# Kernel tuning notes

Measured on AMD Instinct MI355X. Metric: run time of the kernel, lower is better.

## Reference

```python
import jax, jax.numpy as jnp
import numpy as np

V, E, TH, SRC = 50000, 128, 512, 512
B, S, OOV = 256, 512, 100
UNK = 1
NEG_INF = jnp.float32(-jnp.inf)


def setup_inputs() -> dict:
    key = jax.random.key(0)
    ks = jax.random.split(key, 16)
    sc = 0.02
    inp = {
        'embedding': jax.random.normal(ks[0], (V, E), jnp.float32) * sc,
        'W_ih': jax.random.normal(ks[1], (4 * TH, E + TH + SRC), jnp.float32) * sc,
        'W_hh': jax.random.normal(ks[2], (4 * TH, TH), jnp.float32) * sc,
        'b_ih': jnp.zeros((4 * TH,), jnp.float32),
        'b_hh': jnp.zeros((4 * TH,), jnp.float32),
        'W_attn': jax.random.normal(ks[3], (SRC, TH), jnp.float32) * sc,
        'W_out': jax.random.normal(ks[4], (TH, SRC + TH), jnp.float32) * sc,
        'b_out': jnp.zeros((TH,), jnp.float32),
        'W_copy': jax.random.normal(ks[5], (TH, SRC), jnp.float32) * sc,
        'W_incopy': jax.random.normal(ks[6], (TH, SRC), jnp.float32) * sc,
        'W_gen': jax.random.normal(ks[7], (V, TH), jnp.float32) * sc,
        'encoder_output': jax.random.normal(ks[8], (B, S, SRC), jnp.float32),
        'prev_context_state': jax.random.normal(ks[9], (B, TH), jnp.float32),
        'h0': jax.random.normal(ks[10], (B, TH), jnp.float32),
        'c0': jax.random.normal(ks[11], (B, TH), jnp.float32),
        'prev_output_tokens': jax.random.randint(ks[12], (B, 1), 0, V, jnp.int64 if jax.config.jax_enable_x64 else jnp.int32),
        'src_tokens_with_oov': jax.random.randint(ks[13], (B, S), 0, V + OOV, jnp.int64 if jax.config.jax_enable_x64 else jnp.int32),
    }
    lengths = jax.random.randint(ks[14], (B, 1), S // 2, S + 1)
    inp['encoder_padding_mask'] = jnp.arange(S)[None, :] >= lengths  # B x S bool
    return inp


def reference(embedding, W_ih, W_hh, b_ih, b_hh, W_attn, W_out, b_out,
              W_copy, W_incopy, W_gen, encoder_output, prev_context_state,
              h0, c0, prev_output_tokens, src_tokens_with_oov, encoder_padding_mask):
    # ---- attentive-read copy state ----
    match = prev_output_tokens == src_tokens_with_oov            # B x S
    maskf = match[..., None].astype(encoder_output.dtype)        # B x S x 1
    agg = jnp.tanh(jnp.einsum('bsd,hd->bsh', maskf * encoder_output, W_incopy))  # B S TH
    has_match = jnp.any(match, axis=1, keepdims=True)            # B x 1
    fill_mask = has_match & match                                # B x S (as in original)
    in_copy_logit = jnp.einsum('bsh,bh->bs', agg, prev_context_state)
    in_copy_logit = jnp.where(fill_mask, NEG_INF, in_copy_logit)
    in_copy_w = jax.nn.softmax(in_copy_logit, axis=1)            # B x S
    copy_state = jnp.einsum('bs,bsd->bd', in_copy_w, encoder_output)  # B x SRC

    # ---- embed prev token (OOV -> UNK) ----
    tok = jnp.where(prev_output_tokens[:, 0] >= V, UNK, prev_output_tokens[:, 0])
    src_embed = embedding[tok]                                   # B x E

    # ---- one-step LSTM (input_feeding) ----
    x = jnp.concatenate([src_embed, prev_context_state, copy_state], axis=-1)
    gates = x @ W_ih.T + b_ih + h0 @ W_hh.T + b_hh               # B x 4TH
    i, f, g, o = jnp.split(gates, 4, axis=-1)
    c1 = jax.nn.sigmoid(f) * c0 + jax.nn.sigmoid(i) * jnp.tanh(g)
    h1 = jax.nn.sigmoid(o) * jnp.tanh(c1)                        # B x TH

    # ---- general attention ----
    q = h1 @ W_attn.T                                            # B x SRC
    attn_logits = jnp.einsum('bd,bsd->bs', q, encoder_output)
    attn_logits = jnp.where(encoder_padding_mask, NEG_INF, attn_logits)
    attn_w = jax.nn.softmax(attn_logits, axis=1)
    context = jnp.einsum('bs,bsd->bd', attn_w, encoder_output)   # B x SRC
    attn_out = jnp.tanh(jnp.concatenate([context, h1], axis=-1) @ W_out.T + b_out)  # B x TH

    # ---- generate + copy distribution ----
    gen_logits = attn_out @ W_gen.T                              # B x V
    gen_logits = jnp.concatenate([gen_logits, jnp.zeros((gen_logits.shape[0], OOV), gen_logits.dtype)], axis=1)
    copy_seq = jnp.einsum('bsh,bh->bs', jnp.tanh(jnp.einsum('bsd,hd->bsh', encoder_output, W_copy)), attn_out)
    copy_seq = jnp.exp(jnp.where(encoder_padding_mask, NEG_INF, copy_seq))  # B x S
    rows = jnp.arange(copy_seq.shape[0])[:, None]
    copy_vocab = jnp.zeros((copy_seq.shape[0], V + OOV), copy_seq.dtype).at[rows, src_tokens_with_oov].add(copy_seq)

    total = jnp.exp(gen_logits) + copy_vocab
    total_prob = jnp.log(total / jnp.sum(total, axis=1, keepdims=True))
    return total_prob, attn_out, h1, c1
```

## Files before the change

### kernel.cpp

```cpp
#include <hip/hip_runtime.h>
#include <hip/hip_bf16.h>
#include <math.h>

#define V_ 50000
#define OOV_ 100
#define VX_ 50100
#define B_ 256
#define S_ 512
#define TH_ 512
#define SRC_ 512
#define KXH 1664

#define ATT_OFF ((size_t)B_ * VX_)
#define H1_OFF (ATT_OFF + (size_t)B_ * TH_)
#define C1_OFF (H1_OFF + (size_t)B_ * TH_)

typedef float f32x4 __attribute__((ext_vector_type(4)));
typedef short s16x8 __attribute__((ext_vector_type(8)));

__device__ __forceinline__ unsigned short f2bf(float f) {
    unsigned int u = __float_as_uint(f);
    u += 0x7FFFu + ((u >> 16) & 1u);
    return (unsigned short)(u >> 16);
}
__device__ __forceinline__ unsigned int pk2bf(float x, float y) {
    __hip_bfloat162 h = __float22bfloat162_rn(make_float2(x, y));
    return *reinterpret_cast<unsigned int*>(&h);
}
__device__ __forceinline__ float fast_tanh(float x) {
    return 1.0f - 2.0f / (__expf(2.0f * x) + 1.0f);
}
__device__ __forceinline__ float sigm(float x) { return 1.0f / (1.0f + __expf(-x)); }

__device__ __forceinline__ bool get_mask(const void* m, int flag, size_t idx) {
    return flag ? (((const unsigned char*)m)[idx] != 0)
                : (((const int*)m)[idx] != 0);
}

__device__ __forceinline__ void mfma_acc(f32x4& c, s16x8 a, s16x8 b) {
    c = __builtin_amdgcn_mfma_f32_16x16x32_bf16(a, b, c, 0, 0, 0);
}


__device__ __forceinline__ void stage_bf16(const unsigned short* src, int ld,
                                           int row0, int k0, unsigned char* ldsbase) {
    const int tid = threadIdx.x;
    const int w = tid >> 6, lane = tid & 63;
#pragma unroll
    for (int jj = 0; jj < 2; ++jj) {
        const int qq = w * 2 + jj;
        const int rowl = qq * 8 + (lane >> 3);
        const int su = (lane & 7) ^ (rowl & 7);
        const unsigned short* g = src + (size_t)(row0 + rowl) * ld + k0 + su * 8;
        __builtin_amdgcn_global_load_lds(
            (const __attribute__((address_space(1))) void*)g,
            (__attribute__((address_space(3))) void*)(ldsbase + qq * 1024), 16, 0, 0);
    }
}

__device__ __forceinline__ void stage_bf16_128(const unsigned short* src, int ld,
                                               int k0, unsigned char* ldsbase) {
    const int tid = threadIdx.x;
    const int w = tid >> 6, lane = tid & 63;
#pragma unroll
    for (int jj = 0; jj < 4; ++jj) {
        const int qq = w * 4 + jj;
        const int rowl = qq * 8 + (lane >> 3);
        const int su = (lane & 7) ^ (rowl & 7);
        const unsigned short* g = src + (size_t)rowl * ld + k0 + su * 8;
        __builtin_amdgcn_global_load_lds(
            (const __attribute__((address_space(1))) void*)g,
            (__attribute__((address_space(3))) void*)(ldsbase + qq * 1024), 16, 0, 0);
    }
}

__device__ __forceinline__ void stage_f32(const float* src, int ld, int row0, int k0,
                                          int rowmax, unsigned char* ldsbase) {
    const int tid = threadIdx.x;
#pragma unroll
    for (int it = 0; it < 4; ++it) {
        const int p = it * 256 + tid;
        const int row = p >> 4;
        const int u4 = p & 15;
        int gr = row0 + row;
        gr = gr > rowmax ? rowmax : gr;
        const float4 v = *(const float4*)(src + (size_t)gr * ld + k0 + u4 * 4);
        *(uint2*)(ldsbase + row * 128 + ((u4 * 8) ^ ((row & 7) << 4))) =
            make_uint2(pk2bf(v.x, v.y), pk2bf(v.z, v.w));
    }
}

__device__ __forceinline__ void compute64(const unsigned char* Ab, const unsigned char* Bb,
                                          f32x4 acc[4]) {
    const int tid = threadIdx.x;
    const int w = tid >> 6, lane = tid & 63, lq = lane >> 4, lr = lane & 15;
#pragma unroll
    for (int ks = 0; ks < 2; ++ks) {
        const int kb = ks * 64 + lq * 16;
        const int ar = w * 16 + lr;
        s16x8 a = *(const s16x8*)(Ab + ar * 128 + (kb ^ ((ar & 7) << 4)));
#pragma unroll
        for (int ns = 0; ns < 4; ++ns) {
            const int br = ns * 16 + lr;
            s16x8 b = *(const s16x8*)(Bb + br * 128 + (kb ^ ((br & 7) << 4)));
            mfma_acc(acc[ns], a, b);
        }
    }
}

template <bool BF32>
__device__ __forceinline__ void gemm_main(const unsigned short* A, int lda, const void* Bp,
                                          int ldb, int nkc, int kbase, int rowmaxB, int m0,
                                          int n0, unsigned char* smem, f32x4 acc[4]) {
#pragma unroll
    for (int i = 0; i < 4; ++i) acc[i] = f32x4{0.f, 0.f, 0.f, 0.f};
    unsigned char* const A0 = smem;
    unsigned char* const B0 = smem + 8192;
    for (int kc = 0; kc < nkc; ++kc) {
        const int k0 = kbase + kc * 64;
        __syncthreads();
        stage_bf16(A, lda, m0, k0, A0);
        if (BF32) stage_f32((const float*)Bp, ldb, n0, k0, rowmaxB, B0);
        else      stage_bf16((const unsigned short*)Bp, ldb, n0, k0, B0);
        __syncthreads();
        compute64(A0, B0, acc);
    }
}


__global__ __launch_bounds__(256) void k_pre(const float* enc, const int* stok, const int* ptok,
                                             float* cs_sum, int* cs_cnt, unsigned short* ebf,
                                             int do_cvt, float* logit, float* rowsum,
                                             const void* maskp, int* flag, float* out,
                                             const float* W_ih, const float* W_hh,
                                             const float* W_copy, unsigned short* Wg,
                                             unsigned short* Wcb, float* gates) {
    const int bid = blockIdx.x, tid = threadIdx.x;
    if (bid < 1024) {
        __shared__ float comb[512];
        __shared__ int cc[2];
        const int b = bid >> 2, chunk = bid & 3;
        const int h = tid >> 7, d0 = (tid & 127) * 4;
        const int prev = ptok[b];
        const float* base = enc + ((size_t)b * S_ + chunk * 128) * SRC_;
        const int* st = stok + b * S_ + chunk * 128;
        unsigned short* eb = ebf + ((size_t)b * S_ + chunk * 128) * SRC_;
        float a0 = 0.f, a1 = 0.f, a2 = 0.f, a3 = 0.f;
        int cnt = 0;
        for (int s2 = 0; s2 < 64; ++s2) {
            const int s = s2 * 2 + h;
            const float4 v = *(const float4*)(base + (size_t)s * SRC_ + d0);
            if (st[s] != prev) { a0 += v.x; a1 += v.y; a2 += v.z; a3 += v.w; ++cnt; }
            if (do_cvt) {
                *(uint2*)(eb + (size_t)s * SRC_ + d0) =
                    make_uint2(pk2bf(v.x, v.y), pk2bf(v.z, v.w));
            }
        }
        if (h == 0) {
            comb[d0] = a0; comb[d0 + 1] = a1; comb[d0 + 2] = a2; comb[d0 + 3] = a3;
            if (tid == 0) cc[0] = cnt;
        }
        __syncthreads();
        if (h == 1) {
            comb[d0] += a0; comb[d0 + 1] += a1; comb[d0 + 2] += a2; comb[d0 + 3] += a3;
            if (tid == 128) cc[1] = cnt;
        }
        __syncthreads();
        cs_sum[(size_t)bid * SRC_ + tid] = comb[tid];
        cs_sum[(size_t)bid * SRC_ + 256 + tid] = comb[256 + tid];
        if (tid == 0) cs_cnt[bid] = cc[0] + cc[1];
    } else if (bid < 1536) {
        logit[(bid - 1024) * 256 + tid] = 0.f;
    } else if (bid == 1536) {
        rowsum[tid] = (float)OOV_;
    } else if (bid == 1537) {
        __shared__ int sfl;
        if (tid == 0) sfl = 0;
        __syncthreads();
        const uint4* m4 = (const uint4*)maskp;
        unsigned int ev = 0;
        for (int i = tid; i < (B_ * S_) / 16; i += 256) {
            const uint4 u = m4[i];
            ev |= (u.x | u.y | u.z | u.w) & 0xFFFFFF00u;
        }
        if (ev) atomicOr(&sfl, 1);
        __syncthreads();
        if (tid == 0) *flag = sfl;
    } else if (bid < 1638) {
        const int p = (bid - 1538) * 256 + tid;
        if (p < B_ * OOV_) {
            const int b = p / OOV_, j = p - b * OOV_;
            out[(size_t)b * VX_ + V_ + j] = 1.0f;
        }
    } else if (bid < 2150) {
        const int NWG = 2048 * KXH;
        const int NTOT4 = (NWG + 512 * 512) / 4;
        for (int i4 = (bid - 1638) * 256 + tid; i4 < NTOT4; i4 += 512 * 256) {
            const int e = i4 * 4;
            float4 v;
            unsigned short* dst;
            if (e < NWG) {
                const int r = e / KXH, c = e - r * KXH;
                v = (c < 1152) ? *(const float4*)(W_ih + (size_t)r * 1152 + c)
                               : *(const float4*)(W_hh + (size_t)r * 512 + (c - 1152));
                dst = Wg + e;
            } else {
                v = *(const float4*)(W_copy + (e - NWG));
                dst = Wcb + (e - NWG);
            }
            *(uint2*)dst = make_uint2(pk2bf(v.x, v.y), pk2bf(v.z, v.w));
        }
    } else {
        ((float4*)gates)[(bid - 2150) * 256 + tid] = make_float4(0.f, 0.f, 0.f, 0.f);
    }
}

__global__ __launch_bounds__(256) void k_cs_final(const float* cs_sum, const int* cs_cnt,
                                                  const float* embedding, const int* ptok,
                                                  const float* pcs, const float* h0,
                                                  unsigned short* xh) {
    const int b = blockIdx.x, tid = threadIdx.x;
    const int cnt = cs_cnt[b * 4] + cs_cnt[b * 4 + 1] + cs_cnt[b * 4 + 2] + cs_cnt[b * 4 + 3];
    const float inv = 1.f / (float)cnt;
    unsigned short* row = xh + (size_t)b * KXH;
    for (int d = tid; d < 512; d += 256) {
        float s = cs_sum[(size_t)(b * 4 + 0) * SRC_ + d] + cs_sum[(size_t)(b * 4 + 1) * SRC_ + d] +
                  cs_sum[(size_t)(b * 4 + 2) * SRC_ + d] + cs_sum[(size_t)(b * 4 + 3) * SRC_ + d];
        row[640 + d] = f2bf(s * inv);
        row[128 + d] = f2bf(pcs[b * 512 + d]);
        row[1152 + d] = f2bf(h0[b * 512 + d]);
    }
    if (tid < 128) {
        int tk = ptok[b];
        if (tk >= V_) tk = 1;
        row[tid] = f2bf(embedding[(size_t)tk * 128 + tid]);
    }
}

__global__ __launch_bounds__(256) void k_gates(const unsigned short* xh, const unsigned short* Wg,
                                               float* gates) {
    __shared__ __align__(16) unsigned char smem[16384];
    f32x4 acc[4];
    const int m0 = blockIdx.x * 64, n0 = blockIdx.y * 64;
    const int kb = blockIdx.z ? 832 : 0;
    gemm_main<false>(xh, KXH, Wg, KXH, 13, kb, 2047, m0, n0, smem, acc);
    const int tid = threadIdx.x, w = tid >> 6, lane = tid & 63, lq = lane >> 4, lr = lane & 15;
#pragma unroll
    for (int ns = 0; ns < 4; ++ns) {
        const int n = n0 + ns * 16 + lr;
#pragma unroll
        for (int r = 0; r < 4; ++r) {
            const int m = m0 + w * 16 + lq * 4 + r;
            atomicAdd(&gates[(size_t)m * 2048 + n], acc[ns][r]);
        }
    }
}

__global__ __launch_bounds__(256) void k_lstm(const float* gates, const float* b_ih,
                                              const float* b_hh, const float* c0, float* out,
                                              unsigned short* h1b) {
    const int idx = blockIdx.x * 256 + threadIdx.x;
    const int b = idx >> 9, h = idx & 511;
    const float gi = gates[(size_t)b * 2048 + h] + b_ih[h] + b_hh[h];
    const float gf = gates[(size_t)b * 2048 + 512 + h] + b_ih[512 + h] + b_hh[512 + h];
    const float gg = gates[(size_t)b * 2048 + 1024 + h] + b_ih[1024 + h] + b_hh[1024 + h];
    const float go = gates[(size_t)b * 2048 + 1536 + h] + b_ih[1536 + h] + b_hh[1536 + h];
    const float c1 = sigm(gf) * c0[idx] + sigm(gi) * fast_tanh(gg);
    const float h1 = sigm(go) * fast_tanh(c1);
    out[H1_OFF + idx] = h1;
    out[C1_OFF + idx] = c1;
    h1b[idx] = f2bf(h1);
}

__global__ __launch_bounds__(256) void k_q(const unsigned short* h1b, const float* W_attn,
                                           float* qbuf) {
    __shared__ __align__(16) unsigned char smem[16384];
    f32x4 acc[4];
    const int m0 = blockIdx.x * 64, n0 = blockIdx.y * 64;
    gemm_main<true>(h1b, 512, W_attn, 512, 8, 0, 511, m0, n0, smem, acc);
    const int tid = threadIdx.x, w = tid >> 6, lane = tid & 63, lq = lane >> 4, lr = lane & 15;
#pragma unroll
    for (int ns = 0; ns < 4; ++ns) {
        const int n = n0 + ns * 16 + lr;
#pragma unroll
        for (int r = 0; r < 4; ++r)
            qbuf[(size_t)(m0 + w * 16 + lq * 4 + r) * 512 + n] = acc[ns][r];
    }
}

__global__ __launch_bounds__(256) void k_attn2(const float* enc, const unsigned short* ebf,
                                               const int use_ebf, const float* qv,
                                               const void* maskp, const int* flagp,
                                               float* parts, float* md) {
    const int chunk = blockIdx.x, b = blockIdx.y;
    const int tid = threadIdx.x, w = tid >> 6, lane = tid & 63;
    const int flag = *flagp;
    float q0[8];
    {
        const float4 t0 = *(const float4*)(qv + b * 512 + lane * 8);
        const float4 t1 = *(const float4*)(qv + b * 512 + lane * 8 + 4);
        q0[0] = t0.x; q0[1] = t0.y; q0[2] = t0.z; q0[3] = t0.w;
        q0[4] = t1.x; q0[5] = t1.y; q0[6] = t1.z; q0[7] = t1.w;
    }
    float M = -INFINITY, den = 0.f;
    float cv[8] = {0.f, 0.f, 0.f, 0.f, 0.f, 0.f, 0.f, 0.f};
    const int s0 = chunk * 128 + w * 32;
    for (int i = 0; i < 32; ++i) {
        const int s = s0 + i;
        if (get_mask(maskp, flag, (size_t)b * S_ + s)) continue;
        float v[8];
        if (use_ebf) {
            const uint4 u = *(const uint4*)(ebf + ((size_t)b * S_ + s) * 512 + lane * 8);
            v[0] = __uint_as_float(u.x << 16);
            v[1] = __uint_as_float(u.x & 0xffff0000u);
            v[2] = __uint_as_float(u.y << 16);
            v[3] = __uint_as_float(u.y & 0xffff0000u);
            v[4] = __uint_as_float(u.z << 16);
            v[5] = __uint_as_float(u.z & 0xffff0000u);
            v[6] = __uint_as_float(u.w << 16);
            v[7] = __uint_as_float(u.w & 0xffff0000u);
        } else {
            const float4 t0 = *(const float4*)(enc + ((size_t)b * S_ + s) * 512 + lane * 8);
            const float4 t1 = *(const float4*)(enc + ((size_t)b * S_ + s) * 512 + lane * 8 + 4);
            v[0] = t0.x; v[1] = t0.y; v[2] = t0.z; v[3] = t0.w;
            v[4] = t1.x; v[5] = t1.y; v[6] = t1.z; v[7] = t1.w;
        }
        float a = 0.f;
#pragma unroll
        for (int j = 0; j < 8; ++j) a += q0[j] * v[j];
        a += __shfl_xor(a, 1);
        a += __shfl_xor(a, 2);
        a += __shfl_xor(a, 4);
        a += __shfl_xor(a, 8);
        a += __shfl_xor(a, 16);
        a += __shfl_xor(a, 32);
        const float nM = fmaxf(M, a);
        const float sc = __expf(M - nM);
        const float p = __expf(a - nM);
        den = den * sc + p;
#pragma unroll
        for (int j = 0; j < 8; ++j) cv[j] = cv[j] * sc + p * v[j];
        M = nM;
    }
    const int part = chunk * 4 + w;
    float* pp = parts + ((size_t)part * B_ + b) * 512 + lane * 8;
    *(float4*)pp = make_float4(cv[0], cv[1], cv[2], cv[3]);
    *(float4*)(pp + 4) = make_float4(cv[4], cv[5], cv[6], cv[7]);
    if (lane == 0) {
        md[(part * B_ + b) * 2] = M;
        md[(part * B_ + b) * 2 + 1] = den;
    }
}

__global__ __launch_bounds__(256) void k_merge16(const float* parts, const float* md,
                                                 const unsigned short* h1b, unsigned short* ch) {
    const int b = blockIdx.x, tid = threadIdx.x;
    float Ms[16], Ds[16], M = -INFINITY;
#pragma unroll
    for (int jj = 0; jj < 16; ++jj) {
        Ms[jj] = md[(jj * B_ + b) * 2];
        Ds[jj] = md[(jj * B_ + b) * 2 + 1];
        M = fmaxf(M, Ms[jj]);
    }
    float den = 0.f, sc[16];
#pragma unroll
    for (int jj = 0; jj < 16; ++jj) {
        sc[jj] = __expf(Ms[jj] - M);
        den += Ds[jj] * sc[jj];
    }
    const float inv = 1.f / den;
    for (int d = tid; d < 512; d += 256) {
        float c = 0.f;
#pragma unroll
        for (int jj = 0; jj < 16; ++jj) c += parts[((size_t)jj * B_ + b) * 512 + d] * sc[jj];
        ch[(size_t)b * 1024 + d] = f2bf(c * inv);
    }
    ch[(size_t)b * 1024 + 512 + tid] = h1b[b * 512 + tid];
    ch[(size_t)b * 1024 + 512 + 256 + tid] = h1b[b * 512 + 256 + tid];
}

__global__ __launch_bounds__(256) void k_attnout(const unsigned short* ch, const float* W_out,
                                                 const float* b_out, float* out,
                                                 unsigned short* aob) {
    __shared__ __align__(16) unsigned char smem[16384];
    f32x4 acc[4];
    const int m0 = blockIdx.x * 64, n0 = blockIdx.y * 64;
    gemm_main<true>(ch, 1024, W_out, 1024, 16, 0, 511, m0, n0, smem, acc);
    const int tid = threadIdx.x, w = tid >> 6, lane = tid & 63, lq = lane >> 4, lr = lane & 15;
#pragma unroll
    for (int ns = 0; ns < 4; ++ns) {
        const int n = n0 + ns * 16 + lr;
        const float bb = b_out[n];
#pragma unroll
        for (int r = 0; r < 4; ++r) {
            const int m = m0 + w * 16 + lq * 4 + r;
            const float t = fast_tanh(acc[ns][r] + bb);
            out[ATT_OFF + (size_t)m * 512 + n] = t;
            aob[(size_t)m * 512 + n] = f2bf(t);
        }
    }
}

__global__ __launch_bounds__(256) void k_gen(const unsigned short* aob, const float* W_gen,
                                             float* out, float* rowsum) {
    __shared__ __align__(16) unsigned char smem[16384];
    f32x4 acc[4];
    const int d = blockIdx.x;
    const int l = (d & 7) * 391 + (d >> 3);
    const int m0 = (l & 3) * 64;
    const int n0 = (l >> 2) * 64;
    gemm_main<true>(aob, 512, W_gen, 512, 8, 0, V_ - 1, m0, n0, smem, acc);
    const int tid = threadIdx.x, w = tid >> 6, lane = tid & 63, lq = lane >> 4, lr = lane & 15;
    float rp[4] = {0.f, 0.f, 0.f, 0.f};
#pragma unroll
    for (int ns = 0; ns < 4; ++ns) {
        const int n = n0 + ns * 16 + lr;
        if (n < V_) {
#pragma unroll
            for (int r = 0; r < 4; ++r) {
                const float v = __expf(acc[ns][r]);
                out[(size_t)(m0 + w * 16 + lq * 4 + r) * VX_ + n] = v;
                rp[r] += v;
            }
        }
    }
#pragma unroll
    for (int r = 0; r < 4; ++r) {
        rp[r] += __shfl_xor(rp[r], 1, 16);
        rp[r] += __shfl_xor(rp[r], 2, 16);
        rp[r] += __shfl_xor(rp[r], 4, 16);
        rp[r] += __shfl_xor(rp[r], 8, 16);
    }
    if (lr == 0) {
#pragma unroll
        for (int r = 0; r < 4; ++r) atomicAdd(&rowsum[m0 + w * 16 + lq * 4 + r], rp[r]);
    }
}

__global__ __launch_bounds__(256) void k_copyseq_bf(const unsigned short* ebf,
                                                    const unsigned short* Wcb,
                                                    const float* ao, const void* maskp,
                                                    const int* flagp, float* logit) {
    const int d = blockIdx.x;
    const int l = (d & 7) * 512 + (d >> 3);
    const int n0 = (l & 3) * 128;
    const int mt = l >> 2;
    const int m0 = mt * 128;
    const int b = mt >> 2;
    if (get_mask(maskp, *flagp, (size_t)b * S_ + (m0 & 511))) return;
    __shared__ __align__(16) unsigned char smem[65536];
    unsigned char* const A0 = smem;
    unsigned char* const A1 = smem + 16384;
    unsigned char* const B0 = smem + 32768;
    unsigned char* const B1 = smem + 49152;
    const int tid = threadIdx.x;
    const int w = tid >> 6, lane = tid & 63;
    const int wm = w >> 1, wn = w & 1, lq = lane >> 4, lr = lane & 15;
    const unsigned short* Asrc = ebf + (size_t)m0 * 512;
    const unsigned short* Bsrc = Wcb + (size_t)n0 * 512;

    f32x4 acc[4][4];
#pragma unroll
    for (int mi = 0; mi < 4; ++mi)
#pragma unroll
        for (int ni = 0; ni < 4; ++ni) acc[mi][ni] = f32x4{0.f, 0.f, 0.f, 0.f};

    stage_bf16_128(Asrc, 512, 0, A0);
    stage_bf16_128(Bsrc, 512, 0, B0);

    for (int kc = 0; kc < 8; ++kc) {
        __syncthreads();
        const unsigned char* Ac = (kc & 1) ? A1 : A0;
        const unsigned char* Bc = (kc & 1) ? B1 : B0;
        if (kc < 7) {
            stage_bf16_128(Asrc, 512, (kc + 1) * 64, (kc & 1) ? A0 : A1);
            stage_bf16_128(Bsrc, 512, (kc + 1) * 64, (kc & 1) ? B0 : B1);
        }
#pragma unroll
        for (int ks = 0; ks < 2; ++ks) {
            const int kb = ks * 64 + lq * 16;
            s16x8 afr[4], bfr[4];
#pragma unroll
            for (int mi = 0; mi < 4; ++mi) {
                const int ar = wm * 64 + mi * 16 + lr;
                afr[mi] = *(const s16x8*)(Ac + ar * 128 + (kb ^ ((ar & 7) << 4)));
            }
#pragma unroll
            for (int ni = 0; ni < 4; ++ni) {
                const int br = wn * 64 + ni * 16 + lr;
                bfr[ni] = *(const s16x8*)(Bc + br * 128 + (kb ^ ((br & 7) << 4)));
            }
#pragma unroll
            for (int mi = 0; mi < 4; ++mi)
#pragma unroll
                for (int ni = 0; ni < 4; ++ni) mfma_acc(acc[mi][ni], afr[mi], bfr[ni]);
        }
    }

    float aow[4];
#pragma unroll
    for (int ni = 0; ni < 4; ++ni) aow[ni] = ao[b * 512 + n0 + wn * 64 + ni * 16 + lr];
#pragma unroll
    for (int mi = 0; mi < 4; ++mi) {
#pragma unroll
        for (int r = 0; r < 4; ++r) {
            float p = 0.f;
#pragma unroll
            for (int ni = 0; ni < 4; ++ni) p += fast_tanh(acc[mi][ni][r]) * aow[ni];
            p += __shfl_xor(p, 1, 16);
            p += __shfl_xor(p, 2, 16);
            p += __shfl_xor(p, 4, 16);
            p += __shfl_xor(p, 8, 16);
            if (lr == 0)
                atomicAdd(&logit[(size_t)m0 + wm * 64 + mi * 16 + lq * 4 + r], p);
        }
    }
}

__global__ __launch_bounds__(256) void k_copyseq(const float* enc, const unsigned short* Wcb,
                                                 const float* ao, const void* maskp,
                                                 const int* flagp, float* logit) {
    const int m0 = blockIdx.x * 128;
    const int n0 = blockIdx.y * 128;
    const int b = blockIdx.x >> 2;
    if (get_mask(maskp, *flagp, (size_t)b * S_ + (m0 & 511))) return;
    __shared__ __align__(16) unsigned char smem[32768];
    unsigned char* const A0 = smem;
    unsigned char* const B0 = smem + 16384;
    const int tid = threadIdx.x;
    const int w = tid >> 6, lane = tid & 63;
    const int wm = w >> 1, wn = w & 1, lq = lane >> 4, lr = lane & 15;
    const float* Asrc = enc + (size_t)m0 * 512;

    f32x4 acc[4][4];
#pragma unroll
    for (int mi = 0; mi < 4; ++mi)
#pragma unroll
        for (int ni = 0; ni < 4; ++ni) acc[mi][ni] = f32x4{0.f, 0.f, 0.f, 0.f};

    const int arow_t = tid >> 3, au_t = tid & 7;
    for (int kc = 0; kc < 8; ++kc) {
        __syncthreads();
        const int k0 = kc * 64;
#pragma unroll
        for (int it = 0; it < 4; ++it) {
            const int row = arow_t + it * 32;
            const float* g = Asrc + (size_t)row * 512 + k0 + au_t * 8;
            const float4 v0 = *(const float4*)g;
            const float4 v1 = *(const float4*)(g + 4);
            uint4 pk;
            pk.x = pk2bf(v0.x, v0.y);
            pk.y = pk2bf(v0.z, v0.w);
            pk.z = pk2bf(v1.x, v1.y);
            pk.w = pk2bf(v1.z, v1.w);
            *(uint4*)(A0 + row * 128 + ((au_t * 16) ^ ((row & 7) << 4))) = pk;
        }
        stage_bf16_128(Wcb + (size_t)n0 * 512, 512, k0, B0);
        __syncthreads();
#pragma unroll
        for (int ks = 0; ks < 2; ++ks) {
            const int kb = ks * 64 + lq * 16;
            s16x8 afr[4], bfr[4];
#pragma unroll
            for (int mi = 0; mi < 4; ++mi) {
                const int ar = wm * 64 + mi * 16 + lr;
                afr[mi] = *(const s16x8*)(A0 + ar * 128 + (kb ^ ((ar & 7) << 4)));
            }
#pragma unroll
            for (int ni = 0; ni < 4; ++ni) {
                const int br = wn * 64 + ni * 16 + lr;
                bfr[ni] = *(const s16x8*)(B0 + br * 128 + (kb ^ ((br & 7) << 4)));
            }
#pragma unroll
            for (int mi = 0; mi < 4; ++mi)
#pragma unroll
                for (int ni = 0; ni < 4; ++ni) mfma_acc(acc[mi][ni], afr[mi], bfr[ni]);
        }
    }

    float aow[4];
#pragma unroll
    for (int ni = 0; ni < 4; ++ni) aow[ni] = ao[b * 512 + n0 + wn * 64 + ni * 16 + lr];
#pragma unroll
    for (int mi = 0; mi < 4; ++mi) {
#pragma unroll
        for (int r = 0; r < 4; ++r) {
            float p = 0.f;
#pragma unroll
            for (int ni = 0; ni < 4; ++ni) p += fast_tanh(acc[mi][ni][r]) * aow[ni];
            p += __shfl_xor(p, 1, 16);
            p += __shfl_xor(p, 2, 16);
            p += __shfl_xor(p, 4, 16);
            p += __shfl_xor(p, 8, 16);
            if (lr == 0)
                atomicAdd(&logit[(size_t)m0 + wm * 64 + mi * 16 + lq * 4 + r], p);
        }
    }
}

__global__ __launch_bounds__(256) void k_scatter(const float* logit, const int* stok,
                                                 const void* maskp, const int* flagp,
                                                 float* out, float* rowsum) {
    const int idx = blockIdx.x * 256 + threadIdx.x;
    const int b = idx >> 9;
    const int flag = *flagp;
    float v = 0.f;
    if (!get_mask(maskp, flag, idx)) {
        v = __expf(logit[idx]);
        atomicAdd(&out[(size_t)b * VX_ + stok[idx]], v);
    }
    float s = v;
#pragma unroll
    for (int o = 1; o < 64; o <<= 1) s += __shfl_xor(s, o, 64);
    if ((threadIdx.x & 63) == 0) atomicAdd(&rowsum[b], s);
}

__global__ __launch_bounds__(256) void k_final(float* out, const float* rowsum) {
    const int b = blockIdx.y;
    const float ls = __logf(rowsum[b]);
    int v = blockIdx.x * 1024 + threadIdx.x;
#pragma unroll
    for (int i = 0; i < 4; ++i, v += 256) {
        if (v < VX_) {
            const size_t o = (size_t)b * VX_ + v;
            out[o] = __logf(out[o]) - ls;
        }
    }
}


extern "C" void kernel_launch(void* const* d_in, const int* in_sizes, int n_in, void* d_out,
                              int out_size, void* d_ws, size_t ws_size, hipStream_t stream) {
    const float* embedding = (const float*)d_in[0];
    const float* W_ih = (const float*)d_in[1];
    const float* W_hh = (const float*)d_in[2];
    const float* b_ih = (const float*)d_in[3];
    const float* b_hh = (const float*)d_in[4];
    const float* W_attn = (const float*)d_in[5];
    const float* W_out = (const float*)d_in[6];
    const float* b_out = (const float*)d_in[7];
    const float* W_copy = (const float*)d_in[8];
    const float* W_gen = (const float*)d_in[10];
    const float* enc = (const float*)d_in[11];
    const float* pcs = (const float*)d_in[12];
    const float* h0 = (const float*)d_in[13];
    const float* c0 = (const float*)d_in[14];
    const int* ptok = (const int*)d_in[15];
    const int* stok = (const int*)d_in[16];
    const void* maskp = d_in[17];
    float* out = (float*)d_out;

    char* ws = (char*)d_ws;
    size_t off = 0;
    auto alloc = [&](size_t bytes) {
        size_t o = off;
        off += (bytes + 255) & ~(size_t)255;
        return o;
    };
    int* flag = (int*)(ws + alloc(4));
    float* rowsum = (float*)(ws + alloc(B_ * 4));
    float* cs_sum = (float*)(ws + alloc((size_t)1024 * SRC_ * 4));
    int* cs_cnt = (int*)(ws + alloc(1024 * 4));
    unsigned short* xh = (unsigned short*)(ws + alloc((size_t)B_ * KXH * 2));
    unsigned short* Wg = (unsigned short*)(ws + alloc((size_t)2048 * KXH * 2));
    unsigned short* Wcb = (unsigned short*)(ws + alloc((size_t)512 * 512 * 2));
    float* gates = (float*)(ws + alloc((size_t)B_ * 2048 * 4));
    unsigned short* h1b = (unsigned short*)(ws + alloc((size_t)B_ * 512 * 2));
    float* qbuf = (float*)(ws + alloc((size_t)B_ * 512 * 4));
    float* parts = (float*)(ws + alloc((size_t)16 * B_ * 512 * 4));
    float* md = (float*)(ws + alloc((size_t)16 * B_ * 2 * 4));
    unsigned short* ch = (unsigned short*)(ws + alloc((size_t)B_ * 1024 * 2));
    unsigned short* aob = (unsigned short*)(ws + alloc((size_t)B_ * 512 * 2));
    float* logit = (float*)(ws + alloc((size_t)B_ * S_ * 4));
    const size_t ebf_bytes = (size_t)B_ * S_ * SRC_ * 2;
    const int use_ebf = (off + ebf_bytes <= ws_size) ? 1 : 0;
    unsigned short* ebf = (unsigned short*)(ws + off);
    (void)n_in; (void)in_sizes; (void)out_size;

    hipLaunchKernelGGL(k_pre, dim3(2662), dim3(256), 0, stream, enc, stok, ptok, cs_sum, cs_cnt,
                       ebf, use_ebf, logit, rowsum, maskp, flag, out, W_ih, W_hh, W_copy, Wg,
                       Wcb, gates);
    hipLaunchKernelGGL(k_cs_final, dim3(256), dim3(256), 0, stream, cs_sum, cs_cnt, embedding,
                       ptok, pcs, h0, xh);
    hipLaunchKernelGGL(k_gates, dim3(4, 32, 2), dim3(256), 0, stream, xh, Wg, gates);
    hipLaunchKernelGGL(k_lstm, dim3(512), dim3(256), 0, stream, gates, b_ih, b_hh, c0, out, h1b);
    hipLaunchKernelGGL(k_q, dim3(4, 8), dim3(256), 0, stream, h1b, W_attn, qbuf);
    hipLaunchKernelGGL(k_attn2, dim3(4, 256), dim3(256), 0, stream, enc, ebf, use_ebf, qbuf,
                       maskp, flag, parts, md);
    hipLaunchKernelGGL(k_merge16, dim3(256), dim3(256), 0, stream, parts, md, h1b, ch);
    hipLaunchKernelGGL(k_attnout, dim3(4, 8), dim3(256), 0, stream, ch, W_out, b_out, out, aob);
    hipLaunchKernelGGL(k_gen, dim3(3128), dim3(256), 0, stream, aob, W_gen, out, rowsum);
    if (use_ebf) {
        hipLaunchKernelGGL(k_copyseq_bf, dim3(4096), dim3(256), 0, stream, ebf, Wcb,
                           out + ATT_OFF, maskp, flag, logit);
    } else {
        hipLaunchKernelGGL(k_copyseq, dim3(1024, 4), dim3(256), 0, stream, enc, Wcb,
                           out + ATT_OFF, maskp, flag, logit);
    }
    hipLaunchKernelGGL(k_scatter, dim3(512), dim3(256), 0, stream, logit, stok, maskp, flag,
                       out, rowsum);
    hipLaunchKernelGGL(k_final, dim3(49, 256), dim3(256), 0, stream, out, rowsum);
}
```

Baseline: 454.1 us.

## Fuse attention merge into one kernel and co-launch gen and copy GEMMs

Attention read is done by one 1024-thread block per batch row, which merges the 16 partial softmax states in LDS instead of writing partials to global memory and running a separate merge kernel. The generation GEMM and the copy-sequence GEMM are combined into one launch with block-index dispatch so the two can overlap on the GPU. The final log-normalize kernel is vectorized to float4. In exchange, attention parallelism drops to 256 blocks, and all tail blocks reserve 64KB of LDS, which may reduce occupancy for the gen part.

```diff
diff --git a/kernel.cpp b/kernel.cpp
--- a/kernel.cpp
+++ b/kernel.cpp
@@ -288,11 +288,13 @@
     }
 }
 
-__global__ __launch_bounds__(256) void k_attn2(const float* enc, const unsigned short* ebf,
-                                               const int use_ebf, const float* qv,
-                                               const void* maskp, const int* flagp,
-                                               float* parts, float* md) {
-    const int chunk = blockIdx.x, b = blockIdx.y;
+__global__ __launch_bounds__(1024) void k_attn3(const float* enc, const unsigned short* ebf,
+                                                const int use_ebf, const float* qv,
+                                                const void* maskp, const int* flagp,
+                                                const unsigned short* h1b, unsigned short* ch) {
+    __shared__ float plds[16][512];
+    __shared__ float mdl[16][2];
+    const int b = blockIdx.x;
     const int tid = threadIdx.x, w = tid >> 6, lane = tid & 63;
     const int flag = *flagp;
     float q0[8];
@@ -304,7 +306,7 @@
     }
     float M = -INFINITY, den = 0.f;
     float cv[8] = {0.f, 0.f, 0.f, 0.f, 0.f, 0.f, 0.f, 0.f};
-    const int s0 = chunk * 128 + w * 32;
+    const int s0 = w * 32;
     for (int i = 0; i < 32; ++i) {
         const int s = s0 + i;
         if (get_mask(maskp, flag, (size_t)b * S_ + s)) continue;
@@ -342,41 +344,25 @@
         for (int j = 0; j < 8; ++j) cv[j] = cv[j] * sc + p * v[j];
         M = nM;
     }
-    const int part = chunk * 4 + w;
-    float* pp = parts + ((size_t)part * B_ + b) * 512 + lane * 8;
-    *(float4*)pp = make_float4(cv[0], cv[1], cv[2], cv[3]);
-    *(float4*)(pp + 4) = make_float4(cv[4], cv[5], cv[6], cv[7]);
-    if (lane == 0) {
-        md[(part * B_ + b) * 2] = M;
-        md[(part * B_ + b) * 2 + 1] = den;
-    }
-}
-
-__global__ __launch_bounds__(256) void k_merge16(const float* parts, const float* md,
-                                                 const unsigned short* h1b, unsigned short* ch) {
-    const int b = blockIdx.x, tid = threadIdx.x;
-    float Ms[16], Ds[16], M = -INFINITY;
-#pragma unroll
-    for (int jj = 0; jj < 16; ++jj) {
-        Ms[jj] = md[(jj * B_ + b) * 2];
-        Ds[jj] = md[(jj * B_ + b) * 2 + 1];
-        M = fmaxf(M, Ms[jj]);
-    }
-    float den = 0.f, sc[16];
-#pragma unroll
-    for (int jj = 0; jj < 16; ++jj) {
-        sc[jj] = __expf(Ms[jj] - M);
-        den += Ds[jj] * sc[jj];
-    }
-    const float inv = 1.f / den;
-    for (int d = tid; d < 512; d += 256) {
-        float c = 0.f;
-#pragma unroll
-        for (int jj = 0; jj < 16; ++jj) c += parts[((size_t)jj * B_ + b) * 512 + d] * sc[jj];
-        ch[(size_t)b * 1024 + d] = f2bf(c * inv);
-    }
-    ch[(size_t)b * 1024 + 512 + tid] = h1b[b * 512 + tid];
-    ch[(size_t)b * 1024 + 512 + 256 + tid] = h1b[b * 512 + 256 + tid];
+    if (lane == 0) { mdl[w][0] = M; mdl[w][1] = den; }
+    *(float4*)&plds[w][lane * 8] = make_float4(cv[0], cv[1], cv[2], cv[3]);
+    *(float4*)&plds[w][lane * 8 + 4] = make_float4(cv[4], cv[5], cv[6], cv[7]);
+    __syncthreads();
+    if (tid < 512) {
+        float Mg = -INFINITY;
+#pragma unroll
+        for (int j = 0; j < 16; ++j) Mg = fmaxf(Mg, mdl[j][0]);
+        float deng = 0.f, c = 0.f;
+#pragma unroll
+        for (int j = 0; j < 16; ++j) {
+            const float sc = __expf(mdl[j][0] - Mg);
+            deng += mdl[j][1] * sc;
+            c += plds[j][tid] * sc;
+        }
+        ch[(size_t)b * 1024 + tid] = f2bf(c / deng);
+    } else {
+        ch[(size_t)b * 1024 + tid] = h1b[b * 512 + (tid - 512)];
+    }
 }
 
 __global__ __launch_bounds__(256) void k_attnout(const unsigned short* ch, const float* W_out,
@@ -401,118 +387,118 @@
     }
 }
 
-__global__ __launch_bounds__(256) void k_gen(const unsigned short* aob, const float* W_gen,
-                                             float* out, float* rowsum) {
-    __shared__ __align__(16) unsigned char smem[16384];
-    f32x4 acc[4];
-    const int d = blockIdx.x;
-    const int l = (d & 7) * 391 + (d >> 3);
-    const int m0 = (l & 3) * 64;
-    const int n0 = (l >> 2) * 64;
-    gemm_main<true>(aob, 512, W_gen, 512, 8, 0, V_ - 1, m0, n0, smem, acc);
-    const int tid = threadIdx.x, w = tid >> 6, lane = tid & 63, lq = lane >> 4, lr = lane & 15;
-    float rp[4] = {0.f, 0.f, 0.f, 0.f};
-#pragma unroll
-    for (int ns = 0; ns < 4; ++ns) {
-        const int n = n0 + ns * 16 + lr;
-        if (n < V_) {
-#pragma unroll
-            for (int r = 0; r < 4; ++r) {
-                const float v = __expf(acc[ns][r]);
-                out[(size_t)(m0 + w * 16 + lq * 4 + r) * VX_ + n] = v;
-                rp[r] += v;
-            }
-        }
-    }
-#pragma unroll
-    for (int r = 0; r < 4; ++r) {
-        rp[r] += __shfl_xor(rp[r], 1, 16);
-        rp[r] += __shfl_xor(rp[r], 2, 16);
-        rp[r] += __shfl_xor(rp[r], 4, 16);
-        rp[r] += __shfl_xor(rp[r], 8, 16);
-    }
-    if (lr == 0) {
-#pragma unroll
-        for (int r = 0; r < 4; ++r) atomicAdd(&rowsum[m0 + w * 16 + lq * 4 + r], rp[r]);
-    }
-}
-
-__global__ __launch_bounds__(256) void k_copyseq_bf(const unsigned short* ebf,
-                                                    const unsigned short* Wcb,
-                                                    const float* ao, const void* maskp,
-                                                    const int* flagp, float* logit) {
-    const int d = blockIdx.x;
-    const int l = (d & 7) * 512 + (d >> 3);
-    const int n0 = (l & 3) * 128;
-    const int mt = l >> 2;
-    const int m0 = mt * 128;
-    const int b = mt >> 2;
-    if (get_mask(maskp, *flagp, (size_t)b * S_ + (m0 & 511))) return;
+__global__ __launch_bounds__(256) void k_tail(const unsigned short* ebf,
+                                              const unsigned short* Wcb, const float* ao,
+                                              const unsigned short* aob, const float* W_gen,
+                                              const void* maskp, const int* flagp, float* out,
+                                              float* logit, float* rowsum) {
     __shared__ __align__(16) unsigned char smem[65536];
-    unsigned char* const A0 = smem;
-    unsigned char* const A1 = smem + 16384;
-    unsigned char* const B0 = smem + 32768;
-    unsigned char* const B1 = smem + 49152;
     const int tid = threadIdx.x;
     const int w = tid >> 6, lane = tid & 63;
-    const int wm = w >> 1, wn = w & 1, lq = lane >> 4, lr = lane & 15;
-    const unsigned short* Asrc = ebf + (size_t)m0 * 512;
-    const unsigned short* Bsrc = Wcb + (size_t)n0 * 512;
-
-    f32x4 acc[4][4];
-#pragma unroll
-    for (int mi = 0; mi < 4; ++mi)
-#pragma unroll
-        for (int ni = 0; ni < 4; ++ni) acc[mi][ni] = f32x4{0.f, 0.f, 0.f, 0.f};
-
-    stage_bf16_128(Asrc, 512, 0, A0);
-    stage_bf16_128(Bsrc, 512, 0, B0);
-
-    for (int kc = 0; kc < 8; ++kc) {
-        __syncthreads();
-        const unsigned char* Ac = (kc & 1) ? A1 : A0;
-        const unsigned char* Bc = (kc & 1) ? B1 : B0;
-        if (kc < 7) {
-            stage_bf16_128(Asrc, 512, (kc + 1) * 64, (kc & 1) ? A0 : A1);
-            stage_bf16_128(Bsrc, 512, (kc + 1) * 64, (kc & 1) ? B0 : B1);
-        }
-#pragma unroll
-        for (int ks = 0; ks < 2; ++ks) {
-            const int kb = ks * 64 + lq * 16;
-            s16x8 afr[4], bfr[4];
-#pragma unroll
-            for (int mi = 0; mi < 4; ++mi) {
-                const int ar = wm * 64 + mi * 16 + lr;
-                afr[mi] = *(const s16x8*)(Ac + ar * 128 + (kb ^ ((ar & 7) << 4)));
-            }
-#pragma unroll
-            for (int ni = 0; ni < 4; ++ni) {
-                const int br = wn * 64 + ni * 16 + lr;
-                bfr[ni] = *(const s16x8*)(Bc + br * 128 + (kb ^ ((br & 7) << 4)));
-            }
-#pragma unroll
-            for (int mi = 0; mi < 4; ++mi)
-#pragma unroll
-                for (int ni = 0; ni < 4; ++ni) mfma_acc(acc[mi][ni], afr[mi], bfr[ni]);
-        }
-    }
-
-    float aow[4];
-#pragma unroll
-    for (int ni = 0; ni < 4; ++ni) aow[ni] = ao[b * 512 + n0 + wn * 64 + ni * 16 + lr];
-#pragma unroll
-    for (int mi = 0; mi < 4; ++mi) {
+    const int lq = lane >> 4, lr = lane & 15;
+
+    if (blockIdx.x < 4096) {
+        const int d = blockIdx.x;
+        const int l = (d & 7) * 512 + (d >> 3);
+        const int n0 = (l & 3) * 128;
+        const int mt = l >> 2;
+        const int m0 = mt * 128;
+        const int b = mt >> 2;
+        if (get_mask(maskp, *flagp, (size_t)b * S_ + (m0 & 511))) return;
+        unsigned char* const A0 = smem;
+        unsigned char* const A1 = smem + 16384;
+        unsigned char* const B0 = smem + 32768;
+        unsigned char* const B1 = smem + 49152;
+        const int wm = w >> 1, wn = w & 1;
+        const unsigned short* Asrc = ebf + (size_t)m0 * 512;
+        const unsigned short* Bsrc = Wcb + (size_t)n0 * 512;
+
+        f32x4 acc[4][4];
+#pragma unroll
+        for (int mi = 0; mi < 4; ++mi)
+#pragma unroll
+            for (int ni = 0; ni < 4; ++ni) acc[mi][ni] = f32x4{0.f, 0.f, 0.f, 0.f};
+
+        stage_bf16_128(Asrc, 512, 0, A0);
+        stage_bf16_128(Bsrc, 512, 0, B0);
+
+        for (int kc = 0; kc < 8; ++kc) {
+            __syncthreads();
+            const unsigned char* Ac = (kc & 1) ? A1 : A0;
+            const unsigned char* Bc = (kc & 1) ? B1 : B0;
+            if (kc < 7) {
+                stage_bf16_128(Asrc, 512, (kc + 1) * 64, (kc & 1) ? A0 : A1);
+                stage_bf16_128(Bsrc, 512, (kc + 1) * 64, (kc & 1) ? B0 : B1);
+            }
+#pragma unroll
+            for (int ks = 0; ks < 2; ++ks) {
+                const int kb = ks * 64 + lq * 16;
+                s16x8 afr[4], bfr[4];
+#pragma unroll
+                for (int mi = 0; mi < 4; ++mi) {
+                    const int ar = wm * 64 + mi * 16 + lr;
+                    afr[mi] = *(const s16x8*)(Ac + ar * 128 + (kb ^ ((ar & 7) << 4)));
+                }
+#pragma unroll
+                for (int ni = 0; ni < 4; ++ni) {
+                    const int br = wn * 64 + ni * 16 + lr;
+                    bfr[ni] = *(const s16x8*)(Bc + br * 128 + (kb ^ ((br & 7) << 4)));
+                }
+#pragma unroll
+                for (int mi = 0; mi < 4; ++mi)
+#pragma unroll
+                    for (int ni = 0; ni < 4; ++ni) mfma_acc(acc[mi][ni], afr[mi], bfr[ni]);
+            }
+        }
+
+        float aow[4];
+#pragma unroll
+        for (int ni = 0; ni < 4; ++ni) aow[ni] = ao[b * 512 + n0 + wn * 64 + ni * 16 + lr];
+#pragma unroll
+        for (int mi = 0; mi < 4; ++mi) {
+#pragma unroll
+            for (int r = 0; r < 4; ++r) {
+                float p = 0.f;
+#pragma unroll
+                for (int ni = 0; ni < 4; ++ni) p += fast_tanh(acc[mi][ni][r]) * aow[ni];
+                p += __shfl_xor(p, 1, 16);
+                p += __shfl_xor(p, 2, 16);
+                p += __shfl_xor(p, 4, 16);
+                p += __shfl_xor(p, 8, 16);
+                if (lr == 0)
+                    atomicAdd(&logit[(size_t)m0 + wm * 64 + mi * 16 + lq * 4 + r], p);
+            }
+        }
+    } else {
+        const int d = blockIdx.x - 4096;
+        const int l = (d & 7) * 391 + (d >> 3);
+        const int m0 = (l & 3) * 64;
+        const int n0 = (l >> 2) * 64;
+        f32x4 acc[4];
+        gemm_main<true>(aob, 512, W_gen, 512, 8, 0, V_ - 1, m0, n0, smem, acc);
+        float rp[4] = {0.f, 0.f, 0.f, 0.f};
+#pragma unroll
+        for (int ns = 0; ns < 4; ++ns) {
+            const int n = n0 + ns * 16 + lr;
+            if (n < V_) {
+#pragma unroll
+                for (int r = 0; r < 4; ++r) {
+                    const float v = __expf(acc[ns][r]);
+                    out[(size_t)(m0 + w * 16 + lq * 4 + r) * VX_ + n] = v;
+                    rp[r] += v;
+                }
+            }
+        }
 #pragma unroll
         for (int r = 0; r < 4; ++r) {
-            float p = 0.f;
-#pragma unroll
-            for (int ni = 0; ni < 4; ++ni) p += fast_tanh(acc[mi][ni][r]) * aow[ni];
-            p += __shfl_xor(p, 1, 16);
-            p += __shfl_xor(p, 2, 16);
-            p += __shfl_xor(p, 4, 16);
-            p += __shfl_xor(p, 8, 16);
-            if (lr == 0)
-                atomicAdd(&logit[(size_t)m0 + wm * 64 + mi * 16 + lq * 4 + r], p);
+            rp[r] += __shfl_xor(rp[r], 1, 16);
+            rp[r] += __shfl_xor(rp[r], 2, 16);
+            rp[r] += __shfl_xor(rp[r], 4, 16);
+            rp[r] += __shfl_xor(rp[r], 8, 16);
+        }
+        if (lr == 0) {
+#pragma unroll
+            for (int r = 0; r < 4; ++r) atomicAdd(&rowsum[m0 + w * 16 + lq * 4 + r], rp[r]);
         }
     }
 }
@@ -598,6 +584,42 @@
     }
 }
 
+__global__ __launch_bounds__(256) void k_gen(const unsigned short* aob, const float* W_gen,
+                                             float* out, float* rowsum) {
+    __shared__ __align__(16) unsigned char smem[16384];
+    f32x4 acc[4];
+    const int d = blockIdx.x;
+    const int l = (d & 7) * 391 + (d >> 3);
+    const int m0 = (l & 3) * 64;
+    const int n0 = (l >> 2) * 64;
+    gemm_main<true>(aob, 512, W_gen, 512, 8, 0, V_ - 1, m0, n0, smem, acc);
+    const int tid = threadIdx.x, w = tid >> 6, lane = tid & 63, lq = lane >> 4, lr = lane & 15;
+    float rp[4] = {0.f, 0.f, 0.f, 0.f};
+#pragma unroll
+    for (int ns = 0; ns < 4; ++ns) {
+        const int n = n0 + ns * 16 + lr;
+        if (n < V_) {
+#pragma unroll
+            for (int r = 0; r < 4; ++r) {
+                const float v = __expf(acc[ns][r]);
+                out[(size_t)(m0 + w * 16 + lq * 4 + r) * VX_ + n] = v;
+                rp[r] += v;
+            }
+        }
+    }
+#pragma unroll
+    for (int r = 0; r < 4; ++r) {
+        rp[r] += __shfl_xor(rp[r], 1, 16);
+        rp[r] += __shfl_xor(rp[r], 2, 16);
+        rp[r] += __shfl_xor(rp[r], 4, 16);
+        rp[r] += __shfl_xor(rp[r], 8, 16);
+    }
+    if (lr == 0) {
+#pragma unroll
+        for (int r = 0; r < 4; ++r) atomicAdd(&rowsum[m0 + w * 16 + lq * 4 + r], rp[r]);
+    }
+}
+
 __global__ __launch_bounds__(256) void k_scatter(const float* logit, const int* stok,
                                                  const void* maskp, const int* flagp,
                                                  float* out, float* rowsum) {
@@ -618,13 +640,15 @@
 __global__ __launch_bounds__(256) void k_final(float* out, const float* rowsum) {
     const int b = blockIdx.y;
     const float ls = __logf(rowsum[b]);
-    int v = blockIdx.x * 1024 + threadIdx.x;
-#pragma unroll
-    for (int i = 0; i < 4; ++i, v += 256) {
-        if (v < VX_) {
-            const size_t o = (size_t)b * VX_ + v;
-            out[o] = __logf(out[o]) - ls;
-        }
+    const int p = blockIdx.x * 256 + threadIdx.x;
+    if (p < 12525) {
+        float4* o4 = (float4*)(out + (size_t)b * VX_) + p;
+        float4 v = *o4;
+        v.x = __logf(v.x) - ls;
+        v.y = __logf(v.y) - ls;
+        v.z = __logf(v.z) - ls;
+        v.w = __logf(v.w) - ls;
+        *o4 = v;
     }
 }
 
@@ -667,8 +691,6 @@
     float* gates = (float*)(ws + alloc((size_t)B_ * 2048 * 4));
     unsigned short* h1b = (unsigned short*)(ws + alloc((size_t)B_ * 512 * 2));
     float* qbuf = (float*)(ws + alloc((size_t)B_ * 512 * 4));
-    float* parts = (float*)(ws + alloc((size_t)16 * B_ * 512 * 4));
-    float* md = (float*)(ws + alloc((size_t)16 * B_ * 2 * 4));
     unsigned short* ch = (unsigned short*)(ws + alloc((size_t)B_ * 1024 * 2));
     unsigned short* aob = (unsigned short*)(ws + alloc((size_t)B_ * 512 * 2));
     float* logit = (float*)(ws + alloc((size_t)B_ * S_ * 4));
@@ -685,15 +707,14 @@
     hipLaunchKernelGGL(k_gates, dim3(4, 32, 2), dim3(256), 0, stream, xh, Wg, gates);
     hipLaunchKernelGGL(k_lstm, dim3(512), dim3(256), 0, stream, gates, b_ih, b_hh, c0, out, h1b);
     hipLaunchKernelGGL(k_q, dim3(4, 8), dim3(256), 0, stream, h1b, W_attn, qbuf);
-    hipLaunchKernelGGL(k_attn2, dim3(4, 256), dim3(256), 0, stream, enc, ebf, use_ebf, qbuf,
-                       maskp, flag, parts, md);
-    hipLaunchKernelGGL(k_merge16, dim3(256), dim3(256), 0, stream, parts, md, h1b, ch);
+    hipLaunchKernelGGL(k_attn3, dim3(256), dim3(1024), 0, stream, enc, ebf, use_ebf, qbuf,
+                       maskp, flag, h1b, ch);
     hipLaunchKernelGGL(k_attnout, dim3(4, 8), dim3(256), 0, stream, ch, W_out, b_out, out, aob);
-    hipLaunchKernelGGL(k_gen, dim3(3128), dim3(256), 0, stream, aob, W_gen, out, rowsum);
     if (use_ebf) {
-        hipLaunchKernelGGL(k_copyseq_bf, dim3(4096), dim3(256), 0, stream, ebf, Wcb,
-                           out + ATT_OFF, maskp, flag, logit);
+        hipLaunchKernelGGL(k_tail, dim3(7224), dim3(256), 0, stream, ebf, Wcb, out + ATT_OFF,
+                           aob, W_gen, maskp, flag, out, logit, rowsum);
     } else {
+        hipLaunchKernelGGL(k_gen, dim3(3128), dim3(256), 0, stream, aob, W_gen, out, rowsum);
         hipLaunchKernelGGL(k_copyseq, dim3(1024, 4), dim3(256), 0, stream, enc, Wcb,
                            out + ATT_OFF, maskp, flag, logit);
     }
```

Result: faster. 427.1 us (-5.9%).
